# Optimization experiments

Hardware: AMD Instinct MI355X
Metric: run time of the kernel (lower is better)

Reference implementation:

```python
import jax, jax.numpy as jnp
import numpy as np

H = 64          # hidden_dim
N = 40000       # nodes
E = 60000       # edges  -> 2E edge rows
C5 = 30000      # 5-cycles -> 5*C5 rows
C6 = 25000      # 6-cycles -> 6*C6 rows
E_ROWS, C5_ROWS, C6_ROWS = 2 * E, 5 * C5, 6 * C6
EPS = 1e-5


def setup_inputs() -> dict:
    key = jax.random.key(0)
    ks = jax.random.split(key, 10)
    d = {}
    d["edge_feats"] = jax.random.normal(ks[0], (E_ROWS, H), jnp.float32)
    d["cycle5_feats"] = jax.random.normal(ks[1], (C5_ROWS, H), jnp.float32)
    d["cycle6_feats"] = jax.random.normal(ks[2], (C6_ROWS, H), jnp.float32)
    d["edge_atoms"] = jax.random.randint(ks[3], (E_ROWS,), 0, N, jnp.int32)
    d["cycle5_atoms"] = jax.random.randint(ks[4], (C5_ROWS,), 0, N, jnp.int32)
    d["cycle6_atoms"] = jax.random.randint(ks[5], (C6_ROWS,), 0, N, jnp.int32)
    # edge_mlp: Linear(11H -> 2H, no bias), BN, ReLU, Linear(2H -> H, no bias), BN, ReLU
    d["e_W1"] = jax.random.normal(ks[6], (11 * H, 2 * H), jnp.float32) * 0.05
    d["e_g1"] = jnp.ones((2 * H,), jnp.float32)
    d["e_b1"] = jnp.zeros((2 * H,), jnp.float32)
    d["e_W2"] = jax.random.normal(ks[7], (2 * H, H), jnp.float32) * 0.05
    d["e_g2"] = jnp.ones((H,), jnp.float32)
    d["e_b2"] = jnp.zeros((H,), jnp.float32)
    # cycle_mlp: Linear(5H -> 2H), BN, ReLU, Linear(2H -> H), BN, ReLU
    d["c_W1"] = jax.random.normal(ks[8], (5 * H, 2 * H), jnp.float32) * 0.05
    d["c_g1"] = jnp.ones((2 * H,), jnp.float32)
    d["c_b1"] = jnp.zeros((2 * H,), jnp.float32)
    d["c_W2"] = jax.random.normal(ks[9], (2 * H, H), jnp.float32) * 0.05
    d["c_g2"] = jnp.ones((H,), jnp.float32)
    d["c_b2"] = jnp.zeros((H,), jnp.float32)
    return d


def _bn(x, g, b):
    # BatchNorm1d in training mode: batch statistics over the row dim
    m = jnp.mean(x, axis=0)
    v = jnp.var(x, axis=0)
    return g * (x - m) * jax.lax.rsqrt(v + EPS) + b


def _mlp(x, W1, g1, b1, W2, g2, b2):
    h = jax.nn.relu(_bn(x @ W1, g1, b1))
    return jax.nn.relu(_bn(h @ W2, g2, b2))


def _gather1(src, src_atoms, tgt_atoms, tgt_seg, n_tgt):
    # order-1 -> order-1 gather_from_ptensors: channels double
    # local map: per-node accumulation of source rows, read back at target atoms
    node = jax.ops.segment_sum(src, src_atoms, num_segments=N)   # [N, c]
    local = node[tgt_atoms]                                      # [R_tgt, c]
    # broadcast map: reduce over target reference domain, broadcast to its rows
    bc = jax.ops.segment_sum(local, tgt_seg, num_segments=n_tgt)[tgt_seg]
    return jnp.concatenate([local, bc], axis=-1)                 # [R_tgt, 2c]


def reference(edge_feats, cycle5_feats, cycle6_feats,
              edge_atoms, cycle5_atoms, cycle6_atoms,
              e_W1, e_g1, e_b1, e_W2, e_g2, e_b2,
              c_W1, c_g1, c_b1, c_W2, c_g2, c_b2):
    e_seg = jnp.repeat(jnp.arange(E), 2)
    c5_seg = jnp.repeat(jnp.arange(C5), 5)
    c6_seg = jnp.repeat(jnp.arange(C6), 6)

    # edge -> cycle gather, then cycle -> cycle gather (h -> 2h -> 4h)
    e2c5 = _gather1(edge_feats, edge_atoms, cycle5_atoms, c5_seg, C5)
    e2c5 = _gather1(e2c5, cycle5_atoms, cycle5_atoms, c5_seg, C5)
    e2c6 = _gather1(edge_feats, edge_atoms, cycle6_atoms, c6_seg, C6)
    e2c6 = _gather1(e2c6, cycle6_atoms, cycle6_atoms, c6_seg, C6)

    # cat_channels with cycle reps (4h + h = 5h)
    new5 = jnp.concatenate([e2c5, cycle5_feats], axis=-1)
    new6 = jnp.concatenate([e2c6, cycle6_feats], axis=-1)

    # cycle -> edge gathers, summed (5h -> 10h)
    c2e = (_gather1(new5, cycle5_atoms, edge_atoms, e_seg, E)
           + _gather1(new6, cycle6_atoms, edge_atoms, e_seg, E))

    edge_out = _mlp(jnp.concatenate([edge_feats, c2e], axis=-1),
                    e_W1, e_g1, e_b1, e_W2, e_g2, e_b2)
    cycle5_out = _mlp(new5, c_W1, c_g1, c_b1, c_W2, c_g2, c_b2)
    cycle6_out = _mlp(new6, c_W1, c_g1, c_b1, c_W2, c_g2, c_b2)
    return (edge_out, cycle5_out, cycle6_out)
```

## Files before the change

kernel.cpp:

```cpp
#include <hip/hip_runtime.h>
#include <hip/hip_bf16.h>

#define NNODES 40000
#define NEDGE  60000
#define NCYC5  30000
#define NCYC6  25000
#define EROWS  (2*NEDGE)
#define C5ROWS (5*NCYC5)
#define C6ROWS (6*NCYC6)

typedef __attribute__((ext_vector_type(8))) short short8;
typedef __attribute__((ext_vector_type(4))) float f32x4;

__device__ __forceinline__ short f2bs(float x){
  union { __hip_bfloat16 h; short s; } u; u.h = __float2bfloat16(x); return u.s;
}
__device__ __forceinline__ float bs2f(short s){
  union { short s; __hip_bfloat16 h; } u; u.s = s; return __bfloat162float(u.h);
}

__device__ __forceinline__ short8 combine_pair(short8 a){
  union U { short8 v; int i[4]; } u, w;
  u.v = a;
  #pragma unroll
  for (int j = 0; j < 4; ++j) w.i[j] = __shfl_xor(u.i[j], 1);
  short8 r;
  #pragma unroll
  for (int j = 0; j < 8; ++j) r[j] = f2bs(bs2f(a[j]) + bs2f(w.v[j]));
  return r;
}

__global__ void hist_k(const int* __restrict__ atoms, int* __restrict__ deg, int n){
  int r = blockIdx.x*256 + threadIdx.x;
  if (r < n) atomicAdd(&deg[atoms[r]], 1);
}

__global__ void scan3_k(const int* __restrict__ d0, const int* __restrict__ d1,
                        const int* __restrict__ d2, int* __restrict__ o0,
                        int* __restrict__ o1, int* __restrict__ o2){
  const int* deg = blockIdx.x==0 ? d0 : (blockIdx.x==1 ? d1 : d2);
  int* offs      = blockIdx.x==0 ? o0 : (blockIdx.x==1 ? o1 : o2);
  const int N = NNODES;
  __shared__ int part[1024];
  int tid = threadIdx.x;
  const int chunk = (N + 1023) / 1024;
  int lo = tid*chunk, hi = min(lo+chunk, N);
  int s = 0;
  for (int i = lo; i < hi; ++i) s += deg[i];
  part[tid] = s;
  __syncthreads();
  for (int d = 1; d < 1024; d <<= 1){
    int v = (tid >= d) ? part[tid-d] : 0;
    __syncthreads();
    part[tid] += v;
    __syncthreads();
  }
  int pref = (tid == 0) ? 0 : part[tid-1];
  for (int i = lo; i < hi; ++i){ offs[i] = pref; pref += deg[i]; }
  if (tid == 1023) offs[N] = part[1023];
}

__global__ void fill_k(const int* __restrict__ atoms, const int* __restrict__ offs,
                       int* __restrict__ cursor, int* __restrict__ rows, int n){
  int r = blockIdx.x*256 + threadIdx.x;
  if (r < n){ int a = atoms[r]; rows[offs[a] + atomicAdd(&cursor[a],1)] = r; }
}

template<int CW, int RDIV, int ACC, int INB, int OUTB>
__global__ void gath_k(const void* __restrict__ srcv, const int* __restrict__ offs,
                       const int* __restrict__ rows, void* __restrict__ dstv,
                       int OS, int OFF){
  int t = blockIdx.x*256 + threadIdx.x;
  if (t >= NNODES*CW) return;
  int n = t / CW, ch = t - n*CW;
  int o = offs[n], e = offs[n+1];
  float s = 0.f;
  for (int i = o; i < e; ++i){
    int r = rows[i];
    size_t si = (size_t)(r / RDIV) * CW + ch;
    s += INB ? bs2f(((const short*)srcv)[si]) : ((const float*)srcv)[si];
  }
  size_t di = (size_t)n*OS + OFF + ch;
  if (OUTB){ short* d = (short*)dstv; d[di] = f2bs((ACC ? bs2f(d[di]) : 0.f) + s); }
  else     { float* d = (float*)dstv; d[di] = (ACC ? d[di] : 0.f) + s; }
}

template<int R>
__global__ void s1_k(const float* __restrict__ node_e, const int* __restrict__ atoms,
                     float* __restrict__ S1, int C){
  int t = blockIdx.x*256 + threadIdx.x;
  if (t >= C*64) return;
  int c = t >> 6, ch = t & 63;
  const int* ap = atoms + c*R;
  float s = 0.f;
  #pragma unroll
  for (int j = 0; j < R; ++j) s += node_e[(size_t)ap[j]*64 + ch];
  S1[t] = s;
}

__global__ void n5lo_k(const float* __restrict__ node_e, const int* __restrict__ offs,
                       short* __restrict__ n5h){
  int t = blockIdx.x*256 + threadIdx.x;
  if (t >= NNODES*64) return;
  int n = t >> 6, ch = t & 63;
  float d = (float)(offs[n+1] - offs[n]);
  n5h[(size_t)n*128 + ch] = f2bs(d * node_e[(size_t)n*64 + ch]);
}

template<int R>
__global__ void s2_k(const short* __restrict__ n5h, const int* __restrict__ atoms,
                     short* __restrict__ S2h, int C){
  int t = blockIdx.x*256 + threadIdx.x;
  if (t >= C*128) return;
  int c = t >> 7, ch = t & 127;
  const int* ap = atoms + c*R;
  float s = 0.f;
  #pragma unroll
  for (int j = 0; j < R; ++j) s += bs2f(n5h[(size_t)ap[j]*128 + ch]);
  S2h[t] = f2bs(s);
}

__global__ void nc0_k(const short* __restrict__ n5, const short* __restrict__ n6,
                      const int* __restrict__ o5, const int* __restrict__ o6,
                      short* __restrict__ nodeC){
  int t = blockIdx.x*256 + threadIdx.x;
  if (t >= NNODES*128) return;
  int n = t >> 7;
  float d5 = (float)(o5[n+1]-o5[n]), d6 = (float)(o6[n+1]-o6[n]);
  nodeC[(size_t)n*320 + (t & 127)] = f2bs(d5*bs2f(n5[t]) + d6*bs2f(n6[t]));
}

__global__ void f2h_k(const float* __restrict__ src, short* __restrict__ dst, int n4){
  int t = blockIdx.x*256 + threadIdx.x;
  if (t >= n4) return;
  float4 v = ((const float4*)src)[t];
  short4 o; o.x=f2bs(v.x); o.y=f2bs(v.y); o.z=f2bs(v.z); o.w=f2bs(v.w);
  ((short4*)dst)[t] = o;
}

__global__ void tr_k(const float* __restrict__ W, short* __restrict__ WT, int K, int logN){
  int t = blockIdx.x*256 + threadIdx.x;
  if (t >= (K << logN)) return;
  int k = t >> logN, n = t & ((1<<logN)-1);
  WT[(size_t)n*K + k] = f2bs(W[t]);
}

__global__ void mkscale_k(const float* __restrict__ ssum, const float* __restrict__ ssq,
                          const float* __restrict__ g, const float* __restrict__ b,
                          float* __restrict__ scale, float* __restrict__ shift, int M){
  int ch = threadIdx.x;
  float inv  = 1.f / (float)M;
  float mean = ssum[ch]*inv;
  float var  = fmaxf(ssq[ch]*inv - mean*mean, 0.f);
  float sc   = g[ch] * rsqrtf(var + 1e-5f);
  scale[ch] = sc; shift[ch] = b[ch] - mean*sc;
}

__global__ void bnf_k(float* __restrict__ X, const float* __restrict__ ssum,
                      const float* __restrict__ ssq, const float* __restrict__ g,
                      const float* __restrict__ b, int M){
  int t = blockIdx.x*256 + threadIdx.x;
  if (t >= M*64) return;
  int ch = t & 63;
  float inv  = 1.f / (float)M;
  float mean = ssum[ch]*inv;
  float var  = fmaxf(ssq[ch]*inv - mean*mean, 0.f);
  float sc   = g[ch] * rsqrtf(var + 1e-5f);
  X[t] = fmaxf(sc*X[t] + (b[ch] - mean*sc), 0.f);
}

template<int LOADER, int NT, int OUTF32, int KC, int RDIV>
__global__ __launch_bounds__(256) void gemm_k(
    const short* __restrict__ A, const short* __restrict__ G0,
    const short* __restrict__ G1, const float* __restrict__ F0,
    const float* __restrict__ F1, const int* __restrict__ atoms,
    const short* __restrict__ BT, void* __restrict__ CoutV,
    float* __restrict__ ssum, float* __restrict__ ssq, int M)
{
  constexpr int NK = KC/32;
  static_assert(NK % 2 == 0, "final MFMA must read LDS buffer 1 (sred aliases buffer 0)");
  constexpr int NC = NT*16;
  constexpr int CH = (NC*4)/256;
  __shared__ short lds[2*NC*32];

  const int wv   = threadIdx.x >> 6;
  const int lane = threadIdx.x & 63;
  const int row0 = blockIdx.x*64 + wv*16;
  const int l15 = lane & 15, quad = lane >> 4;
  const bool act = (row0 < M);
  const int m = act ? (row0 + l15) : 0;

  int aS = 0, cyc = 0;
  if (LOADER == 1) aS = act ? atoms[m] : 0;
  if (LOADER == 2) { aS = act ? atoms[m] : 0; cyc = m / RDIV; }

  constexpr int NLD = (LOADER==1) ? 12 : (LOADER==2 ? 10 : NK);
  short8 af[NLD];
  if (act) {
    #pragma unroll
    for (int kt = 0; kt < NLD; ++kt) {
      const int k0 = kt*32 + quad*8;
      if (LOADER == 1) {
        if (kt < 2) af[kt] = *reinterpret_cast<const short8*>(A + (size_t)m*64 + k0);
        else        af[kt] = *reinterpret_cast<const short8*>(G0 + (size_t)aS*320 + (k0-64));
      } else if (LOADER == 2) {
        if (kt < 4)      af[kt] = *reinterpret_cast<const short8*>(G0 + (size_t)aS*128 + k0);
        else if (kt < 8) af[kt] = *reinterpret_cast<const short8*>(G1 + (size_t)cyc*128 + (k0-128));
        else             af[kt] = *reinterpret_cast<const short8*>(A + (size_t)m*64 + (k0-256));
      } else {
        af[kt] = *reinterpret_cast<const short8*>(A + (size_t)m*KC + k0);
      }
    }
  }

  auto stage_load = [&](int kt, short8* r){
    #pragma unroll
    for (int i = 0; i < CH; ++i) {
      int id = i*256 + (int)threadIdx.x;
      r[i] = *reinterpret_cast<const short8*>(BT + (size_t)(id>>2)*KC + kt*32 + (id&3)*8);
    }
  };
  auto stage_write = [&](int b, short8* r){
    #pragma unroll
    for (int i = 0; i < CH; ++i) {
      int id = i*256 + (int)threadIdx.x;
      int n = id>>2, c = id&3;
      *reinterpret_cast<short8*>(&lds[b*NC*32 + n*32 + ((c ^ ((n>>1)&3)))*8]) = r[i];
    }
  };

  f32x4 acc[NT];
  #pragma unroll
  for (int nt = 0; nt < NT; ++nt) acc[nt] = (f32x4){0.f,0.f,0.f,0.f};

  short8 sr0[CH], sr1[CH], sr2[CH];
  stage_load(0, sr0);
  if (NK > 1) stage_load(1, sr1);

  #pragma unroll
  for (int kt = 0; kt < NK; ++kt) {
    short8* cur = (kt % 3 == 0) ? sr0 : ((kt % 3 == 1) ? sr1 : sr2);
    stage_write(kt & 1, cur);
    if (kt + 2 < NK) {
      short8* nxt = ((kt+2) % 3 == 0) ? sr0 : (((kt+2) % 3 == 1) ? sr1 : sr2);
      stage_load(kt + 2, nxt);
    }
    __syncthreads();

    if (act) {
      const int k0 = kt*32 + quad*8;
      short8 afk;
      {
        short8 base = af[(kt < NLD) ? kt : (kt - 10)];
        if (LOADER == 3) {
          float sc[8], sh[8];
          const float4* sp = reinterpret_cast<const float4*>(F0 + k0);
          const float4* hp = reinterpret_cast<const float4*>(F1 + k0);
          *reinterpret_cast<float4*>(&sc[0]) = sp[0]; *reinterpret_cast<float4*>(&sc[4]) = sp[1];
          *reinterpret_cast<float4*>(&sh[0]) = hp[0]; *reinterpret_cast<float4*>(&sh[4]) = hp[1];
          #pragma unroll
          for (int j = 0; j < 8; ++j) afk[j] = f2bs(fmaxf(sc[j]*bs2f(base[j]) + sh[j], 0.f));
        } else if (LOADER == 1 && kt >= 12) {
          afk = combine_pair(base);
        } else {
          afk = base;
        }
      }
      #pragma unroll
      for (int nt = 0; nt < NT; ++nt) {
        const int n = nt*16 + l15;
        const short8 bfg = *reinterpret_cast<const short8*>(
            &lds[(kt&1)*NC*32 + n*32 + ((quad ^ ((n>>1)&3)))*8]);
        acc[nt] = __builtin_amdgcn_mfma_f32_16x16x32_bf16(afk, bfg, acc[nt], 0, 0, 0);
      }
    }
  }

  float* sred = reinterpret_cast<float*>(lds);

  #pragma unroll
  for (int nt = 0; nt < NT; ++nt) {
    float ps = 0.f, pq = 0.f;
    if (act) {
      #pragma unroll
      for (int rg = 0; rg < 4; ++rg) {
        float v = acc[nt][rg];
        int r = row0 + quad*4 + rg;
        if (OUTF32) ((float*)CoutV)[(size_t)r*NC + nt*16 + l15] = v;
        else        ((short*)CoutV)[(size_t)r*NC + nt*16 + l15] = f2bs(v);
        ps += v; pq += v*v;
      }
    }
    ps += __shfl_xor(ps, 16); pq += __shfl_xor(pq, 16);
    ps += __shfl_xor(ps, 32); pq += __shfl_xor(pq, 32);
    if (lane < 16) {
      sred[wv*NC + nt*16 + lane]        = ps;
      sred[4*NC + wv*NC + nt*16 + lane] = pq;
    }
  }
  __syncthreads();
  for (int ch = threadIdx.x; ch < NC; ch += 256) {
    float s = sred[ch] + sred[NC + ch] + sred[2*NC + ch] + sred[3*NC + ch];
    float q = sred[4*NC + ch] + sred[5*NC + ch] + sred[6*NC + ch] + sred[7*NC + ch];
    atomicAdd(&ssum[ch], s);
    atomicAdd(&ssq[ch], q);
  }
}

static inline int cdiv(int a, int b){ return (a + b - 1)/b; }

extern "C" void kernel_launch(void* const* d_in, const int* in_sizes, int n_in,
                              void* d_out, int out_size, void* d_ws, size_t ws_size,
                              hipStream_t stream)
{
  const float* edge_feats = (const float*)d_in[0];
  const float* c5_feats   = (const float*)d_in[1];
  const float* c6_feats   = (const float*)d_in[2];
  const int*   e_atoms    = (const int*)d_in[3];
  const int*   c5_atoms   = (const int*)d_in[4];
  const int*   c6_atoms   = (const int*)d_in[5];
  const float* eW1 = (const float*)d_in[6];
  const float* eg1 = (const float*)d_in[7];
  const float* eb1 = (const float*)d_in[8];
  const float* eW2 = (const float*)d_in[9];
  const float* eg2 = (const float*)d_in[10];
  const float* eb2 = (const float*)d_in[11];
  const float* cW1 = (const float*)d_in[12];
  const float* cg1 = (const float*)d_in[13];
  const float* cb1 = (const float*)d_in[14];
  const float* cW2 = (const float*)d_in[15];
  const float* cg2 = (const float*)d_in[16];
  const float* cb2 = (const float*)d_in[17];
  float* out = (float*)d_out;
  (void)in_sizes; (void)n_in; (void)out_size; (void)ws_size;

  char* w = (char*)d_ws;
  auto alloc = [&](size_t bytes) -> char* {
    char* p = w; w += (bytes + 255) & ~(size_t)255; return p;
  };

  char* zbase = w;
  int*  deg_e = (int*)alloc(NNODES*4);
  int*  deg_5 = (int*)alloc(NNODES*4);
  int*  deg_6 = (int*)alloc(NNODES*4);
  int*  cur_e = (int*)alloc(NNODES*4);
  int*  cur_5 = (int*)alloc(NNODES*4);
  int*  cur_6 = (int*)alloc(NNODES*4);
  float* stats = (float*)alloc(1152*4);
  size_t zbytes = (size_t)(w - zbase);

  float* se1 = stats;        float* qe1 = stats + 128;
  float* se2 = stats + 256;  float* qe2 = stats + 320;
  float* s51 = stats + 384;  float* q51 = stats + 512;
  float* s52 = stats + 640;  float* q52 = stats + 704;
  float* s61 = stats + 768;  float* q61 = stats + 896;
  float* s62 = stats + 1024; float* q62 = stats + 1088;

  int* offs_e = (int*)alloc((NNODES+1)*4);
  int* offs_5 = (int*)alloc((NNODES+1)*4);
  int* offs_6 = (int*)alloc((NNODES+1)*4);
  int* rows_e = (int*)alloc((size_t)EROWS*4);
  int* rows_5 = (int*)alloc((size_t)C5ROWS*4);
  int* rows_6 = (int*)alloc((size_t)C6ROWS*4);
  short* nodeC_h = (short*)alloc((size_t)NNODES*320*2);
  short* n5_5h   = (short*)alloc((size_t)NNODES*128*2);
  short* n5_6h   = (short*)alloc((size_t)NNODES*128*2);
  short* S2_5h   = (short*)alloc((size_t)NCYC5*128*2);
  short* S2_6h   = (short*)alloc((size_t)NCYC6*128*2);
  short* ef_h    = (short*)alloc((size_t)EROWS*64*2);
  short* c5f_h   = (short*)alloc((size_t)C5ROWS*64*2);
  short* c6f_h   = (short*)alloc((size_t)C6ROWS*64*2);
  short* eW1T    = (short*)alloc((size_t)128*704*2);
  short* cW1T    = (short*)alloc((size_t)128*320*2);
  short* eW2T    = (short*)alloc((size_t)64*128*2);
  short* cW2T    = (short*)alloc((size_t)64*128*2);
  float* scsh    = (float*)alloc(768*4);
  float* sc_e = scsh;       float* sh_e = scsh + 128;
  float* sc_5 = scsh + 256; float* sh_5 = scsh + 384;
  float* sc_6 = scsh + 512; float* sh_6 = scsh + 640;
  char*  h1reg = alloc((size_t)C5ROWS*128*2);
  short* h1    = (short*)h1reg;
  float* node_e = (float*)h1reg;
  float* S1_5   = (float*)(h1reg + (size_t)NNODES*64*4);
  float* S1_6   = (float*)(h1reg + (size_t)NNODES*64*4 + (size_t)NCYC5*64*4);

  hipMemsetAsync(zbase, 0, zbytes, stream);

  hist_k<<<cdiv(EROWS,256),256,0,stream>>>(e_atoms, deg_e, EROWS);
  hist_k<<<cdiv(C5ROWS,256),256,0,stream>>>(c5_atoms, deg_5, C5ROWS);
  hist_k<<<cdiv(C6ROWS,256),256,0,stream>>>(c6_atoms, deg_6, C6ROWS);
  scan3_k<<<3,1024,0,stream>>>(deg_e, deg_5, deg_6, offs_e, offs_5, offs_6);
  fill_k<<<cdiv(EROWS,256),256,0,stream>>>(e_atoms, offs_e, cur_e, rows_e, EROWS);
  fill_k<<<cdiv(C5ROWS,256),256,0,stream>>>(c5_atoms, offs_5, cur_5, rows_5, C5ROWS);
  fill_k<<<cdiv(C6ROWS,256),256,0,stream>>>(c6_atoms, offs_6, cur_6, rows_6, C6ROWS);

  f2h_k<<<cdiv(EROWS*16,256),256,0,stream>>>(edge_feats, ef_h, EROWS*16);
  f2h_k<<<cdiv(C5ROWS*16,256),256,0,stream>>>(c5_feats, c5f_h, C5ROWS*16);
  f2h_k<<<cdiv(C6ROWS*16,256),256,0,stream>>>(c6_feats, c6f_h, C6ROWS*16);

  gath_k<64,1,0,0,0><<<cdiv(NNODES*64,256),256,0,stream>>>(edge_feats, offs_e, rows_e, node_e, 64, 0);
  s1_k<5><<<cdiv(NCYC5*64,256),256,0,stream>>>(node_e, c5_atoms, S1_5, NCYC5);
  s1_k<6><<<cdiv(NCYC6*64,256),256,0,stream>>>(node_e, c6_atoms, S1_6, NCYC6);
  n5lo_k<<<cdiv(NNODES*64,256),256,0,stream>>>(node_e, offs_5, n5_5h);
  n5lo_k<<<cdiv(NNODES*64,256),256,0,stream>>>(node_e, offs_6, n5_6h);
  gath_k<64,5,0,0,1><<<cdiv(NNODES*64,256),256,0,stream>>>(S1_5, offs_5, rows_5, n5_5h, 128, 64);
  gath_k<64,6,0,0,1><<<cdiv(NNODES*64,256),256,0,stream>>>(S1_6, offs_6, rows_6, n5_6h, 128, 64);
  s2_k<5><<<cdiv(NCYC5*128,256),256,0,stream>>>(n5_5h, c5_atoms, S2_5h, NCYC5);
  s2_k<6><<<cdiv(NCYC6*128,256),256,0,stream>>>(n5_6h, c6_atoms, S2_6h, NCYC6);
  nc0_k<<<cdiv(NNODES*128,256),256,0,stream>>>(n5_5h, n5_6h, offs_5, offs_6, nodeC_h);
  gath_k<128,5,0,1,1><<<cdiv(NNODES*128,256),256,0,stream>>>(S2_5h, offs_5, rows_5, nodeC_h, 320, 128);
  gath_k<128,6,1,1,1><<<cdiv(NNODES*128,256),256,0,stream>>>(S2_6h, offs_6, rows_6, nodeC_h, 320, 128);
  gath_k<64,1,0,0,1><<<cdiv(NNODES*64,256),256,0,stream>>>(c5_feats, offs_5, rows_5, nodeC_h, 320, 256);
  gath_k<64,1,1,0,1><<<cdiv(NNODES*64,256),256,0,stream>>>(c6_feats, offs_6, rows_6, nodeC_h, 320, 256);

  tr_k<<<cdiv(704*128,256),256,0,stream>>>(eW1, eW1T, 704, 7);
  tr_k<<<cdiv(320*128,256),256,0,stream>>>(cW1, cW1T, 320, 7);
  tr_k<<<cdiv(128*64,256),256,0,stream>>>(eW2, eW2T, 128, 6);
  tr_k<<<cdiv(128*64,256),256,0,stream>>>(cW2, cW2T, 128, 6);

  float* out_e = out;
  float* out_5 = out + (size_t)EROWS*64;
  float* out_6 = out + (size_t)(EROWS + C5ROWS)*64;

  gemm_k<1,8,0,704,1><<<cdiv(EROWS,64),256,0,stream>>>(ef_h, nodeC_h, nullptr, nullptr, nullptr,
                                                       e_atoms, eW1T, h1, se1, qe1, EROWS);
  mkscale_k<<<1,128,0,stream>>>(se1, qe1, eg1, eb1, sc_e, sh_e, EROWS);
  gemm_k<3,4,1,128,1><<<cdiv(EROWS,64),256,0,stream>>>(h1, nullptr, nullptr, sc_e, sh_e,
                                                       nullptr, eW2T, out_e, se2, qe2, EROWS);
  bnf_k<<<cdiv(EROWS*64,256),256,0,stream>>>(out_e, se2, qe2, eg2, eb2, EROWS);

  gemm_k<2,8,0,320,5><<<cdiv(C5ROWS,64),256,0,stream>>>(c5f_h, n5_5h, S2_5h, nullptr, nullptr,
                                                        c5_atoms, cW1T, h1, s51, q51, C5ROWS);
  mkscale_k<<<1,128,0,stream>>>(s51, q51, cg1, cb1, sc_5, sh_5, C5ROWS);
  gemm_k<3,4,1,128,1><<<cdiv(C5ROWS,64),256,0,stream>>>(h1, nullptr, nullptr, sc_5, sh_5,
                                                        nullptr, cW2T, out_5, s52, q52, C5ROWS);
  bnf_k<<<cdiv(C5ROWS*64,256),256,0,stream>>>(out_5, s52, q52, cg2, cb2, C5ROWS);

  gemm_k<2,8,0,320,6><<<cdiv(C6ROWS,64),256,0,stream>>>(c6f_h, n5_6h, S2_6h, nullptr, nullptr,
                                                        c6_atoms, cW1T, h1, s61, q61, C6ROWS);
  mkscale_k<<<1,128,0,stream>>>(s61, q61, cg1, cb1, sc_6, sh_6, C6ROWS);
  gemm_k<3,4,1,128,1><<<cdiv(C6ROWS,64),256,0,stream>>>(h1, nullptr, nullptr, sc_6, sh_6,
                                                        nullptr, cW2T, out_6, s62, q62, C6ROWS);
  bnf_k<<<cdiv(C6ROWS*64,256),256,0,stream>>>(out_6, s62, q62, cg2, cb2, C6ROWS);
}
```

Measured before the change: 1.036 ms.

## Merge preprocessing launches, fuse gathers, drop LDS staging in GEMM

Several per-type kernels (histogram, fill, fp32-to-bf16 conversion, weight transposes) are merged into single launches, and the chain of gather, s1 and s2 kernels is fused into fewer per-node and per-cycle kernels. The separate BN scale/shift kernel is removed: the second GEMM now computes mean, variance and scale from the raw sums inline. The GEMM no longer stages B tiles through LDS with double buffering; each wave reads B fragments directly from global memory. Fewer launches and intermediate round-trips are traded for redundant per-lane BN math and uncached, uncoalesced B reads in the GEMM.

```diff
diff --git a/kernel.cpp b/kernel.cpp
--- a/kernel.cpp
+++ b/kernel.cpp
@@ -30,9 +30,13 @@
   return r;
 }
 
-__global__ void hist_k(const int* __restrict__ atoms, int* __restrict__ deg, int n){
+__global__ void hist3_k(const int* __restrict__ ea, const int* __restrict__ c5a,
+                        const int* __restrict__ c6a, int* __restrict__ de,
+                        int* __restrict__ d5, int* __restrict__ d6){
   int r = blockIdx.x*256 + threadIdx.x;
-  if (r < n) atomicAdd(&deg[atoms[r]], 1);
+  if (r < EROWS)                        atomicAdd(&de[ea[r]], 1);
+  else if (r < EROWS + C5ROWS)          atomicAdd(&d5[c5a[r - EROWS]], 1);
+  else if (r < EROWS + C5ROWS + C6ROWS) atomicAdd(&d6[c6a[r - EROWS - C5ROWS]], 1);
 }
 
 __global__ void scan3_k(const int* __restrict__ d0, const int* __restrict__ d1,
@@ -60,100 +64,158 @@
   if (tid == 1023) offs[N] = part[1023];
 }
 
-__global__ void fill_k(const int* __restrict__ atoms, const int* __restrict__ offs,
-                       int* __restrict__ cursor, int* __restrict__ rows, int n){
+__global__ void fill3_k(const int* __restrict__ ea, const int* __restrict__ c5a,
+                        const int* __restrict__ c6a,
+                        const int* __restrict__ oe, const int* __restrict__ o5,
+                        const int* __restrict__ o6,
+                        int* __restrict__ cue, int* __restrict__ cu5,
+                        int* __restrict__ cu6,
+                        int* __restrict__ re, int* __restrict__ r5,
+                        int* __restrict__ r6){
   int r = blockIdx.x*256 + threadIdx.x;
-  if (r < n){ int a = atoms[r]; rows[offs[a] + atomicAdd(&cursor[a],1)] = r; }
-}
-
-template<int CW, int RDIV, int ACC, int INB, int OUTB>
-__global__ void gath_k(const void* __restrict__ srcv, const int* __restrict__ offs,
-                       const int* __restrict__ rows, void* __restrict__ dstv,
-                       int OS, int OFF){
-  int t = blockIdx.x*256 + threadIdx.x;
-  if (t >= NNODES*CW) return;
-  int n = t / CW, ch = t - n*CW;
+  if (r < EROWS){
+    int a = ea[r]; re[oe[a] + atomicAdd(&cue[a],1)] = r;
+  } else if (r < EROWS + C5ROWS){
+    int rr = r - EROWS; int a = c5a[rr]; r5[o5[a] + atomicAdd(&cu5[a],1)] = rr;
+  } else if (r < EROWS + C5ROWS + C6ROWS){
+    int rr = r - EROWS - C5ROWS; int a = c6a[rr]; r6[o6[a] + atomicAdd(&cu6[a],1)] = rr;
+  }
+}
+
+__global__ void gne_k(const float* __restrict__ ef, const int* __restrict__ offs,
+                      const int* __restrict__ rows, float* __restrict__ node_e){
+  int t = blockIdx.x*256 + threadIdx.x;
+  if (t >= NNODES*64) return;
+  int n = t >> 6, ch = t & 63;
   int o = offs[n], e = offs[n+1];
   float s = 0.f;
-  for (int i = o; i < e; ++i){
-    int r = rows[i];
-    size_t si = (size_t)(r / RDIV) * CW + ch;
-    s += INB ? bs2f(((const short*)srcv)[si]) : ((const float*)srcv)[si];
-  }
-  size_t di = (size_t)n*OS + OFF + ch;
-  if (OUTB){ short* d = (short*)dstv; d[di] = f2bs((ACC ? bs2f(d[di]) : 0.f) + s); }
-  else     { float* d = (float*)dstv; d[di] = (ACC ? d[di] : 0.f) + s; }
-}
-
-template<int R>
-__global__ void s1_k(const float* __restrict__ node_e, const int* __restrict__ atoms,
-                     float* __restrict__ S1, int C){
-  int t = blockIdx.x*256 + threadIdx.x;
-  if (t >= C*64) return;
-  int c = t >> 6, ch = t & 63;
-  const int* ap = atoms + c*R;
-  float s = 0.f;
-  #pragma unroll
-  for (int j = 0; j < R; ++j) s += node_e[(size_t)ap[j]*64 + ch];
-  S1[t] = s;
-}
-
-__global__ void n5lo_k(const float* __restrict__ node_e, const int* __restrict__ offs,
-                       short* __restrict__ n5h){
+  for (int i = o; i < e; ++i) s += ef[(size_t)rows[i]*64 + ch];
+  node_e[t] = s;
+}
+
+__global__ void s1f_k(const float* __restrict__ node_e,
+                      const int* __restrict__ a5, const int* __restrict__ a6,
+                      float* __restrict__ S1_5, float* __restrict__ S1_6){
+  int t = blockIdx.x*256 + threadIdx.x;
+  if (t < NCYC5*64){
+    int c = t >> 6, ch = t & 63;
+    const int* ap = a5 + c*5;
+    float s = 0.f;
+    #pragma unroll
+    for (int j = 0; j < 5; ++j) s += node_e[(size_t)ap[j]*64 + ch];
+    S1_5[t] = s;
+  } else if (t < NCYC5*64 + NCYC6*64){
+    int t2 = t - NCYC5*64;
+    int c = t2 >> 6, ch = t2 & 63;
+    const int* ap = a6 + c*6;
+    float s = 0.f;
+    #pragma unroll
+    for (int j = 0; j < 6; ++j) s += node_e[(size_t)ap[j]*64 + ch];
+    S1_6[t2] = s;
+  }
+}
+
+__global__ void n5f_k(const float* __restrict__ node_e,
+                      const int* __restrict__ o5, const int* __restrict__ r5,
+                      const int* __restrict__ o6, const int* __restrict__ r6,
+                      const float* __restrict__ S1_5, const float* __restrict__ S1_6,
+                      short* __restrict__ n5_5h, short* __restrict__ n5_6h){
   int t = blockIdx.x*256 + threadIdx.x;
   if (t >= NNODES*64) return;
   int n = t >> 6, ch = t & 63;
-  float d = (float)(offs[n+1] - offs[n]);
-  n5h[(size_t)n*128 + ch] = f2bs(d * node_e[(size_t)n*64 + ch]);
-}
-
-template<int R>
-__global__ void s2_k(const short* __restrict__ n5h, const int* __restrict__ atoms,
-                     short* __restrict__ S2h, int C){
-  int t = blockIdx.x*256 + threadIdx.x;
-  if (t >= C*128) return;
-  int c = t >> 7, ch = t & 127;
-  const int* ap = atoms + c*R;
-  float s = 0.f;
-  #pragma unroll
-  for (int j = 0; j < R; ++j) s += bs2f(n5h[(size_t)ap[j]*128 + ch]);
-  S2h[t] = f2bs(s);
-}
-
-__global__ void nc0_k(const short* __restrict__ n5, const short* __restrict__ n6,
-                      const int* __restrict__ o5, const int* __restrict__ o6,
+  float v = node_e[t];
+  int a5 = o5[n], b5 = o5[n+1], a6 = o6[n], b6 = o6[n+1];
+  float s5 = 0.f, s6 = 0.f;
+  for (int i = a5; i < b5; ++i) s5 += S1_5[(size_t)(r5[i]/5)*64 + ch];
+  for (int i = a6; i < b6; ++i) s6 += S1_6[(size_t)(r6[i]/6)*64 + ch];
+  n5_5h[(size_t)n*128 + ch]      = f2bs((float)(b5-a5) * v);
+  n5_5h[(size_t)n*128 + 64 + ch] = f2bs(s5);
+  n5_6h[(size_t)n*128 + ch]      = f2bs((float)(b6-a6) * v);
+  n5_6h[(size_t)n*128 + 64 + ch] = f2bs(s6);
+}
+
+__global__ void s2f_k(const short* __restrict__ n5_5h, const short* __restrict__ n5_6h,
+                      const int* __restrict__ a5, const int* __restrict__ a6,
+                      short* __restrict__ S2_5h, short* __restrict__ S2_6h){
+  int t = blockIdx.x*256 + threadIdx.x;
+  if (t < NCYC5*128){
+    int c = t >> 7, ch = t & 127;
+    const int* ap = a5 + c*5;
+    float s = 0.f;
+    #pragma unroll
+    for (int j = 0; j < 5; ++j) s += bs2f(n5_5h[(size_t)ap[j]*128 + ch]);
+    S2_5h[t] = f2bs(s);
+  } else if (t < NCYC5*128 + NCYC6*128){
+    int t2 = t - NCYC5*128;
+    int c = t2 >> 7, ch = t2 & 127;
+    const int* ap = a6 + c*6;
+    float s = 0.f;
+    #pragma unroll
+    for (int j = 0; j < 6; ++j) s += bs2f(n5_6h[(size_t)ap[j]*128 + ch]);
+    S2_6h[t2] = f2bs(s);
+  }
+}
+
+__global__ void ncf_k(const short* __restrict__ n5_5h, const short* __restrict__ n5_6h,
+                      const int* __restrict__ o5, const int* __restrict__ r5,
+                      const int* __restrict__ o6, const int* __restrict__ r6,
+                      const short* __restrict__ S2_5h, const short* __restrict__ S2_6h,
+                      const float* __restrict__ c5f, const float* __restrict__ c6f,
                       short* __restrict__ nodeC){
   int t = blockIdx.x*256 + threadIdx.x;
-  if (t >= NNODES*128) return;
-  int n = t >> 7;
-  float d5 = (float)(o5[n+1]-o5[n]), d6 = (float)(o6[n+1]-o6[n]);
-  nodeC[(size_t)n*320 + (t & 127)] = f2bs(d5*bs2f(n5[t]) + d6*bs2f(n6[t]));
-}
-
-__global__ void f2h_k(const float* __restrict__ src, short* __restrict__ dst, int n4){
-  int t = blockIdx.x*256 + threadIdx.x;
-  if (t >= n4) return;
-  float4 v = ((const float4*)src)[t];
+  if (t >= NNODES*320) return;
+  int n = t / 320, ch = t - n*320;
+  float out;
+  if (ch < 128){
+    float d5 = (float)(o5[n+1]-o5[n]), d6 = (float)(o6[n+1]-o6[n]);
+    out = d5*bs2f(n5_5h[(size_t)n*128 + ch]) + d6*bs2f(n5_6h[(size_t)n*128 + ch]);
+  } else if (ch < 256){
+    int c = ch - 128;
+    float s = 0.f;
+    for (int i = o5[n]; i < o5[n+1]; ++i) s += bs2f(S2_5h[(size_t)(r5[i]/5)*128 + c]);
+    for (int i = o6[n]; i < o6[n+1]; ++i) s += bs2f(S2_6h[(size_t)(r6[i]/6)*128 + c]);
+    out = s;
+  } else {
+    int c = ch - 256;
+    float s = 0.f;
+    for (int i = o5[n]; i < o5[n+1]; ++i) s += c5f[(size_t)r5[i]*64 + c];
+    for (int i = o6[n]; i < o6[n+1]; ++i) s += c6f[(size_t)r6[i]*64 + c];
+    out = s;
+  }
+  nodeC[(size_t)n*320 + ch] = f2bs(out);
+}
+
+__global__ void f2h3_k(const float* __restrict__ e, const float* __restrict__ c5,
+                       const float* __restrict__ c6, short* __restrict__ eh,
+                       short* __restrict__ c5h, short* __restrict__ c6h){
+  int t = blockIdx.x*256 + threadIdx.x;
+  const float* s; short* d; int i;
+  if (t < EROWS*16)                        { s=e;  d=eh;  i=t; }
+  else if (t < EROWS*16 + C5ROWS*16)       { s=c5; d=c5h; i=t - EROWS*16; }
+  else if (t < EROWS*16 + C5ROWS*16 + C6ROWS*16) { s=c6; d=c6h; i=t - EROWS*16 - C5ROWS*16; }
+  else return;
+  float4 v = ((const float4*)s)[i];
   short4 o; o.x=f2bs(v.x); o.y=f2bs(v.y); o.z=f2bs(v.z); o.w=f2bs(v.w);
-  ((short4*)dst)[t] = o;
-}
-
-__global__ void tr_k(const float* __restrict__ W, short* __restrict__ WT, int K, int logN){
-  int t = blockIdx.x*256 + threadIdx.x;
-  if (t >= (K << logN)) return;
-  int k = t >> logN, n = t & ((1<<logN)-1);
-  WT[(size_t)n*K + k] = f2bs(W[t]);
-}
-
-__global__ void mkscale_k(const float* __restrict__ ssum, const float* __restrict__ ssq,
-                          const float* __restrict__ g, const float* __restrict__ b,
-                          float* __restrict__ scale, float* __restrict__ shift, int M){
-  int ch = threadIdx.x;
-  float inv  = 1.f / (float)M;
-  float mean = ssum[ch]*inv;
-  float var  = fmaxf(ssq[ch]*inv - mean*mean, 0.f);
-  float sc   = g[ch] * rsqrtf(var + 1e-5f);
-  scale[ch] = sc; shift[ch] = b[ch] - mean*sc;
+  ((short4*)d)[i] = o;
+}
+
+__global__ void tr4_k(const float* __restrict__ eW1, const float* __restrict__ cW1,
+                      const float* __restrict__ eW2, const float* __restrict__ cW2,
+                      short* __restrict__ eW1T, short* __restrict__ cW1T,
+                      short* __restrict__ eW2T, short* __restrict__ cW2T){
+  int t = blockIdx.x*256 + threadIdx.x;
+  if (t < 704*128){
+    int k = t >> 7, n = t & 127; eW1T[(size_t)n*704 + k] = f2bs(eW1[t]);
+  } else if (t < 704*128 + 320*128){
+    int t2 = t - 704*128; int k = t2 >> 7, n = t2 & 127;
+    cW1T[(size_t)n*320 + k] = f2bs(cW1[t2]);
+  } else if (t < 704*128 + 320*128 + 128*64){
+    int t3 = t - 704*128 - 320*128; int k = t3 >> 6, n = t3 & 63;
+    eW2T[(size_t)n*128 + k] = f2bs(eW2[t3]);
+  } else if (t < 704*128 + 320*128 + 2*128*64){
+    int t4 = t - 704*128 - 320*128 - 128*64; int k = t4 >> 6, n = t4 & 63;
+    cW2T[(size_t)n*128 + k] = f2bs(cW2[t4]);
+  }
 }
 
 __global__ void bnf_k(float* __restrict__ X, const float* __restrict__ ssum,
@@ -178,10 +240,8 @@
     float* __restrict__ ssum, float* __restrict__ ssq, int M)
 {
   constexpr int NK = KC/32;
-  static_assert(NK % 2 == 0, "final MFMA must read LDS buffer 1 (sred aliases buffer 0)");
   constexpr int NC = NT*16;
-  constexpr int CH = (NC*4)/256;
-  __shared__ short lds[2*NC*32];
+  __shared__ float sred[8*NC];
 
   const int wv   = threadIdx.x >> 6;
   const int lane = threadIdx.x & 63;
@@ -194,9 +254,13 @@
   if (LOADER == 1) aS = act ? atoms[m] : 0;
   if (LOADER == 2) { aS = act ? atoms[m] : 0; cyc = m / RDIV; }
 
-  constexpr int NLD = (LOADER==1) ? 12 : (LOADER==2 ? 10 : NK);
-  short8 af[NLD];
+  f32x4 acc[NT];
+  #pragma unroll
+  for (int nt = 0; nt < NT; ++nt) acc[nt] = (f32x4){0.f,0.f,0.f,0.f};
+
   if (act) {
+    constexpr int NLD = (LOADER==1) ? 12 : (LOADER==2 ? 10 : NK);
+    short8 af[NLD];
     #pragma unroll
     for (int kt = 0; kt < NLD; ++kt) {
       const int k0 = kt*32 + quad*8;
@@ -211,55 +275,36 @@
         af[kt] = *reinterpret_cast<const short8*>(A + (size_t)m*KC + k0);
       }
     }
-  }
-
-  auto stage_load = [&](int kt, short8* r){
-    #pragma unroll
-    for (int i = 0; i < CH; ++i) {
-      int id = i*256 + (int)threadIdx.x;
-      r[i] = *reinterpret_cast<const short8*>(BT + (size_t)(id>>2)*KC + kt*32 + (id&3)*8);
-    }
-  };
-  auto stage_write = [&](int b, short8* r){
-    #pragma unroll
-    for (int i = 0; i < CH; ++i) {
-      int id = i*256 + (int)threadIdx.x;
-      int n = id>>2, c = id&3;
-      *reinterpret_cast<short8*>(&lds[b*NC*32 + n*32 + ((c ^ ((n>>1)&3)))*8]) = r[i];
-    }
-  };
-
-  f32x4 acc[NT];
-  #pragma unroll
-  for (int nt = 0; nt < NT; ++nt) acc[nt] = (f32x4){0.f,0.f,0.f,0.f};
-
-  short8 sr0[CH], sr1[CH], sr2[CH];
-  stage_load(0, sr0);
-  if (NK > 1) stage_load(1, sr1);
-
-  #pragma unroll
-  for (int kt = 0; kt < NK; ++kt) {
-    short8* cur = (kt % 3 == 0) ? sr0 : ((kt % 3 == 1) ? sr1 : sr2);
-    stage_write(kt & 1, cur);
-    if (kt + 2 < NK) {
-      short8* nxt = ((kt+2) % 3 == 0) ? sr0 : (((kt+2) % 3 == 1) ? sr1 : sr2);
-      stage_load(kt + 2, nxt);
-    }
-    __syncthreads();
-
-    if (act) {
+
+    const short* bp = BT + (size_t)l15*KC + quad*8;
+    const float invM = 1.f / (float)M;
+
+    #pragma unroll
+    for (int kt = 0; kt < NK; ++kt) {
       const int k0 = kt*32 + quad*8;
       short8 afk;
       {
         short8 base = af[(kt < NLD) ? kt : (kt - 10)];
         if (LOADER == 3) {
-          float sc[8], sh[8];
-          const float4* sp = reinterpret_cast<const float4*>(F0 + k0);
-          const float4* hp = reinterpret_cast<const float4*>(F1 + k0);
-          *reinterpret_cast<float4*>(&sc[0]) = sp[0]; *reinterpret_cast<float4*>(&sc[4]) = sp[1];
-          *reinterpret_cast<float4*>(&sh[0]) = hp[0]; *reinterpret_cast<float4*>(&sh[4]) = hp[1];
+          const float* ssin = reinterpret_cast<const float*>(G0);
+          const float* qqin = reinterpret_cast<const float*>(G1);
+          float ssv[8], qqv[8], gv[8], bv[8];
+          *reinterpret_cast<float4*>(&ssv[0]) = *reinterpret_cast<const float4*>(ssin + k0);
+          *reinterpret_cast<float4*>(&ssv[4]) = *reinterpret_cast<const float4*>(ssin + k0 + 4);
+          *reinterpret_cast<float4*>(&qqv[0]) = *reinterpret_cast<const float4*>(qqin + k0);
+          *reinterpret_cast<float4*>(&qqv[4]) = *reinterpret_cast<const float4*>(qqin + k0 + 4);
+          *reinterpret_cast<float4*>(&gv[0])  = *reinterpret_cast<const float4*>(F0 + k0);
+          *reinterpret_cast<float4*>(&gv[4])  = *reinterpret_cast<const float4*>(F0 + k0 + 4);
+          *reinterpret_cast<float4*>(&bv[0])  = *reinterpret_cast<const float4*>(F1 + k0);
+          *reinterpret_cast<float4*>(&bv[4])  = *reinterpret_cast<const float4*>(F1 + k0 + 4);
           #pragma unroll
-          for (int j = 0; j < 8; ++j) afk[j] = f2bs(fmaxf(sc[j]*bs2f(base[j]) + sh[j], 0.f));
+          for (int j = 0; j < 8; ++j) {
+            float mean = ssv[j]*invM;
+            float var  = fmaxf(qqv[j]*invM - mean*mean, 0.f);
+            float sc   = gv[j] * rsqrtf(var + 1e-5f);
+            float sh   = bv[j] - mean*sc;
+            afk[j] = f2bs(fmaxf(sc*bs2f(base[j]) + sh, 0.f));
+          }
         } else if (LOADER == 1 && kt >= 12) {
           afk = combine_pair(base);
         } else {
@@ -268,15 +313,11 @@
       }
       #pragma unroll
       for (int nt = 0; nt < NT; ++nt) {
-        const int n = nt*16 + l15;
-        const short8 bfg = *reinterpret_cast<const short8*>(
-            &lds[(kt&1)*NC*32 + n*32 + ((quad ^ ((n>>1)&3)))*8]);
+        const short8 bfg = *reinterpret_cast<const short8*>(bp + (size_t)nt*16*KC + kt*32);
         acc[nt] = __builtin_amdgcn_mfma_f32_16x16x32_bf16(afk, bfg, acc[nt], 0, 0, 0);
       }
     }
   }
-
-  float* sred = reinterpret_cast<float*>(lds);
 
   #pragma unroll
   for (int nt = 0; nt < NT; ++nt) {
@@ -374,10 +415,6 @@
   short* cW1T    = (short*)alloc((size_t)128*320*2);
   short* eW2T    = (short*)alloc((size_t)64*128*2);
   short* cW2T    = (short*)alloc((size_t)64*128*2);
-  float* scsh    = (float*)alloc(768*4);
-  float* sc_e = scsh;       float* sh_e = scsh + 128;
-  float* sc_5 = scsh + 256; float* sh_5 = scsh + 384;
-  float* sc_6 = scsh + 512; float* sh_6 = scsh + 640;
   char*  h1reg = alloc((size_t)C5ROWS*128*2);
   short* h1    = (short*)h1reg;
   float* node_e = (float*)h1reg;
@@ -386,37 +423,31 @@
 
   hipMemsetAsync(zbase, 0, zbytes, stream);
 
-  hist_k<<<cdiv(EROWS,256),256,0,stream>>>(e_atoms, deg_e, EROWS);
-  hist_k<<<cdiv(C5ROWS,256),256,0,stream>>>(c5_atoms, deg_5, C5ROWS);
-  hist_k<<<cdiv(C6ROWS,256),256,0,stream>>>(c6_atoms, deg_6, C6ROWS);
+  const int TOTROWS = EROWS + C5ROWS + C6ROWS;
+  hist3_k<<<cdiv(TOTROWS,256),256,0,stream>>>(e_atoms, c5_atoms, c6_atoms,
+                                              deg_e, deg_5, deg_6);
   scan3_k<<<3,1024,0,stream>>>(deg_e, deg_5, deg_6, offs_e, offs_5, offs_6);
-  fill_k<<<cdiv(EROWS,256),256,0,stream>>>(e_atoms, offs_e, cur_e, rows_e, EROWS);
-  fill_k<<<cdiv(C5ROWS,256),256,0,stream>>>(c5_atoms, offs_5, cur_5, rows_5, C5ROWS);
-  fill_k<<<cdiv(C6ROWS,256),256,0,stream>>>(c6_atoms, offs_6, cur_6, rows_6, C6ROWS);
-
-  f2h_k<<<cdiv(EROWS*16,256),256,0,stream>>>(edge_feats, ef_h, EROWS*16);
-  f2h_k<<<cdiv(C5ROWS*16,256),256,0,stream>>>(c5_feats, c5f_h, C5ROWS*16);
-  f2h_k<<<cdiv(C6ROWS*16,256),256,0,stream>>>(c6_feats, c6f_h, C6ROWS*16);
-
-  gath_k<64,1,0,0,0><<<cdiv(NNODES*64,256),256,0,stream>>>(edge_feats, offs_e, rows_e, node_e, 64, 0);
-  s1_k<5><<<cdiv(NCYC5*64,256),256,0,stream>>>(node_e, c5_atoms, S1_5, NCYC5);
-  s1_k<6><<<cdiv(NCYC6*64,256),256,0,stream>>>(node_e, c6_atoms, S1_6, NCYC6);
-  n5lo_k<<<cdiv(NNODES*64,256),256,0,stream>>>(node_e, offs_5, n5_5h);
-  n5lo_k<<<cdiv(NNODES*64,256),256,0,stream>>>(node_e, offs_6, n5_6h);
-  gath_k<64,5,0,0,1><<<cdiv(NNODES*64,256),256,0,stream>>>(S1_5, offs_5, rows_5, n5_5h, 128, 64);
-  gath_k<64,6,0,0,1><<<cdiv(NNODES*64,256),256,0,stream>>>(S1_6, offs_6, rows_6, n5_6h, 128, 64);
-  s2_k<5><<<cdiv(NCYC5*128,256),256,0,stream>>>(n5_5h, c5_atoms, S2_5h, NCYC5);
-  s2_k<6><<<cdiv(NCYC6*128,256),256,0,stream>>>(n5_6h, c6_atoms, S2_6h, NCYC6);
-  nc0_k<<<cdiv(NNODES*128,256),256,0,stream>>>(n5_5h, n5_6h, offs_5, offs_6, nodeC_h);
-  gath_k<128,5,0,1,1><<<cdiv(NNODES*128,256),256,0,stream>>>(S2_5h, offs_5, rows_5, nodeC_h, 320, 128);
-  gath_k<128,6,1,1,1><<<cdiv(NNODES*128,256),256,0,stream>>>(S2_6h, offs_6, rows_6, nodeC_h, 320, 128);
-  gath_k<64,1,0,0,1><<<cdiv(NNODES*64,256),256,0,stream>>>(c5_feats, offs_5, rows_5, nodeC_h, 320, 256);
-  gath_k<64,1,1,0,1><<<cdiv(NNODES*64,256),256,0,stream>>>(c6_feats, offs_6, rows_6, nodeC_h, 320, 256);
-
-  tr_k<<<cdiv(704*128,256),256,0,stream>>>(eW1, eW1T, 704, 7);
-  tr_k<<<cdiv(320*128,256),256,0,stream>>>(cW1, cW1T, 320, 7);
-  tr_k<<<cdiv(128*64,256),256,0,stream>>>(eW2, eW2T, 128, 6);
-  tr_k<<<cdiv(128*64,256),256,0,stream>>>(cW2, cW2T, 128, 6);
+  fill3_k<<<cdiv(TOTROWS,256),256,0,stream>>>(e_atoms, c5_atoms, c6_atoms,
+                                              offs_e, offs_5, offs_6,
+                                              cur_e, cur_5, cur_6,
+                                              rows_e, rows_5, rows_6);
+
+  f2h3_k<<<cdiv((EROWS+C5ROWS+C6ROWS)*16,256),256,0,stream>>>(
+      edge_feats, c5_feats, c6_feats, ef_h, c5f_h, c6f_h);
+  tr4_k<<<cdiv(704*128 + 320*128 + 2*128*64,256),256,0,stream>>>(
+      eW1, cW1, eW2, cW2, eW1T, cW1T, eW2T, cW2T);
+
+  gne_k<<<cdiv(NNODES*64,256),256,0,stream>>>(edge_feats, offs_e, rows_e, node_e);
+  s1f_k<<<cdiv(NCYC5*64 + NCYC6*64,256),256,0,stream>>>(node_e, c5_atoms, c6_atoms,
+                                                        S1_5, S1_6);
+  n5f_k<<<cdiv(NNODES*64,256),256,0,stream>>>(node_e, offs_5, rows_5, offs_6, rows_6,
+                                              S1_5, S1_6, n5_5h, n5_6h);
+  s2f_k<<<cdiv(NCYC5*128 + NCYC6*128,256),256,0,stream>>>(n5_5h, n5_6h,
+                                                          c5_atoms, c6_atoms,
+                                                          S2_5h, S2_6h);
+  ncf_k<<<cdiv(NNODES*320,256),256,0,stream>>>(n5_5h, n5_6h, offs_5, rows_5,
+                                               offs_6, rows_6, S2_5h, S2_6h,
+                                               c5_feats, c6_feats, nodeC_h);
 
   float* out_e = out;
   float* out_5 = out + (size_t)EROWS*64;
@@ -424,22 +455,22 @@
 
   gemm_k<1,8,0,704,1><<<cdiv(EROWS,64),256,0,stream>>>(ef_h, nodeC_h, nullptr, nullptr, nullptr,
                                                        e_atoms, eW1T, h1, se1, qe1, EROWS);
-  mkscale_k<<<1,128,0,stream>>>(se1, qe1, eg1, eb1, sc_e, sh_e, EROWS);
-  gemm_k<3,4,1,128,1><<<cdiv(EROWS,64),256,0,stream>>>(h1, nullptr, nullptr, sc_e, sh_e,
-                                                       nullptr, eW2T, out_e, se2, qe2, EROWS);
+  gemm_k<3,4,1,128,1><<<cdiv(EROWS,64),256,0,stream>>>(h1, (const short*)se1, (const short*)qe1,
+                                                       eg1, eb1, nullptr, eW2T, out_e,
+                                                       se2, qe2, EROWS);
   bnf_k<<<cdiv(EROWS*64,256),256,0,stream>>>(out_e, se2, qe2, eg2, eb2, EROWS);
 
   gemm_k<2,8,0,320,5><<<cdiv(C5ROWS,64),256,0,stream>>>(c5f_h, n5_5h, S2_5h, nullptr, nullptr,
                                                         c5_atoms, cW1T, h1, s51, q51, C5ROWS);
-  mkscale_k<<<1,128,0,stream>>>(s51, q51, cg1, cb1, sc_5, sh_5, C5ROWS);
-  gemm_k<3,4,1,128,1><<<cdiv(C5ROWS,64),256,0,stream>>>(h1, nullptr, nullptr, sc_5, sh_5,
-                                                        nullptr, cW2T, out_5, s52, q52, C5ROWS);
+  gemm_k<3,4,1,128,1><<<cdiv(C5ROWS,64),256,0,stream>>>(h1, (const short*)s51, (const short*)q51,
+                                                        cg1, cb1, nullptr, cW2T, out_5,
+                                                        s52, q52, C5ROWS);
   bnf_k<<<cdiv(C5ROWS*64,256),256,0,stream>>>(out_5, s52, q52, cg2, cb2, C5ROWS);
 
   gemm_k<2,8,0,320,6><<<cdiv(C6ROWS,64),256,0,stream>>>(c6f_h, n5_6h, S2_6h, nullptr, nullptr,
                                                         c6_atoms, cW1T, h1, s61, q61, C6ROWS);
-  mkscale_k<<<1,128,0,stream>>>(s61, q61, cg1, cb1, sc_6, sh_6, C6ROWS);
-  gemm_k<3,4,1,128,1><<<cdiv(C6ROWS,64),256,0,stream>>>(h1, nullptr, nullptr, sc_6, sh_6,
-                                                        nullptr, cW2T, out_6, s62, q62, C6ROWS);
+  gemm_k<3,4,1,128,1><<<cdiv(C6ROWS,64),256,0,stream>>>(h1, (const short*)s61, (const short*)q61,
+                                                        cg1, cb1, nullptr, cW2T, out_6,
+                                                        s62, q62, C6ROWS);
   bnf_k<<<cdiv(C6ROWS*64,256),256,0,stream>>>(out_6, s62, q62, cg2, cb2, C6ROWS);
 }
```

Result: slower. 1.161 ms (+12.0%).
